# Kernel optimization log

Hardware: AMD Instinct MI355X
Metric: run time of the kernel (lower is better)

## Reference

```python
import jax, jax.numpy as jnp
import numpy as np

NEG_SLOPE = 0.2  # PyG GATConv default negative_slope


def gat_conv(x, edge_index, W, att_src, att_dst, bias):
    """PyG-style GATConv (concat heads, add_self_loops=True, eval mode).
    x: [N, F_in], edge_index: [2, E] (row 0 = src j, row 1 = dst i).
    W: [F_in, H*C], att_src/att_dst: [H, C], bias: [H*C].
    """
    N = x.shape[0]
    H, C = att_src.shape
    loops = jnp.arange(N, dtype=edge_index.dtype)
    src = jnp.concatenate([edge_index[0], loops])  # [E+N]
    dst = jnp.concatenate([edge_index[1], loops])
    h = (x @ W).reshape(N, H, C)                              # [N,H,C]
    a_src = jnp.einsum('nhc,hc->nh', h, att_src)              # [N,H]
    a_dst = jnp.einsum('nhc,hc->nh', h, att_dst)
    alpha = jax.nn.leaky_relu(a_src[src] + a_dst[dst], NEG_SLOPE)  # [E+N,H]
    # segment softmax over edges sharing the same destination node
    m = jax.ops.segment_max(alpha, dst, num_segments=N)       # [N,H]
    e = jnp.exp(alpha - jax.lax.stop_gradient(m)[dst])
    denom = jax.ops.segment_sum(e, dst, num_segments=N)       # [N,H]
    a = e / (denom[dst] + 1e-16)                              # [E+N,H]
    msg = h[src] * a[:, :, None]                              # [E+N,H,C]
    out = jax.ops.segment_sum(msg, dst, num_segments=N)       # [N,H,C]
    return out.reshape(N, H * C) + bias


def setup_inputs() -> dict:
    key = jax.random.key(0)
    ks = jax.random.split(key, 10)
    N, F, NC, C1, H1 = 50000, 128, 40, 16, 8
    E = 800000
    x = jax.random.normal(ks[0], (N, F), dtype=jnp.float32)
    edge_index = jax.random.randint(ks[1], (2, E), 0, N, dtype=jnp.int64)
    s1 = 1.0 / np.sqrt(F)
    W1 = jax.random.uniform(ks[2], (F, H1 * C1), jnp.float32, -s1, s1)
    att_src1 = jax.random.uniform(ks[3], (H1, C1), jnp.float32, -1.0, 1.0) * s1
    att_dst1 = jax.random.uniform(ks[4], (H1, C1), jnp.float32, -1.0, 1.0) * s1
    bias1 = jnp.zeros((H1 * C1,), jnp.float32)
    s2 = 1.0 / np.sqrt(H1 * C1)
    W2 = jax.random.uniform(ks[5], (H1 * C1, NC), jnp.float32, -s2, s2)
    att_src2 = jax.random.uniform(ks[6], (1, NC), jnp.float32, -1.0, 1.0) * s2
    att_dst2 = jax.random.uniform(ks[7], (1, NC), jnp.float32, -1.0, 1.0) * s2
    bias2 = jnp.zeros((NC,), jnp.float32)
    return {"x": x, "edge_index": edge_index, "W1": W1, "att_src1": att_src1,
            "att_dst1": att_dst1, "bias1": bias1, "W2": W2, "att_src2": att_src2,
            "att_dst2": att_dst2, "bias2": bias2}


def reference(x, edge_index, W1, att_src1, att_dst1, bias1, W2, att_src2, att_dst2, bias2):
    h = gat_conv(x, edge_index, W1, att_src1, att_dst1, bias1)   # [N, 128]
    # dropout in eval mode = identity
    out = gat_conv(h, edge_index, W2, att_src2, att_dst2, bias2)  # [N, 40]
    return out
```

## Files before the change

kernel.cpp:

```cpp
#include <hip/hip_runtime.h>
#include <hip/hip_bf16.h>
#include <math.h>

#define NEG_SLOPE 0.2f

typedef __bf16 bf16x8 __attribute__((ext_vector_type(8)));
typedef float f32x4 __attribute__((ext_vector_type(4)));

__device__ __forceinline__ float lrelu(float x) { return x > 0.f ? x : NEG_SLOPE * x; }

__device__ __forceinline__ unsigned int pack_bf2(float a, float b) {
    unsigned int ua = __float_as_uint(a);
    ua = (ua + 0x7fffu + ((ua >> 16) & 1u)) >> 16;
    unsigned int ub = __float_as_uint(b);
    ub = (ub + 0x7fffu + ((ub >> 16) & 1u)) & 0xffff0000u;
    return ua | ub;
}
__device__ __forceinline__ unsigned short f2bfu(float f) {
    unsigned int ua = __float_as_uint(f);
    return (unsigned short)((ua + 0x7fffu + ((ua >> 16) & 1u)) >> 16);
}
__device__ __forceinline__ float bf_lo(unsigned int u) { return __uint_as_float(u << 16); }
__device__ __forceinline__ float bf_hi(unsigned int u) { return __uint_as_float(u & 0xffff0000u); }

__global__ __launch_bounds__(256) void k_hist(const int* __restrict__ ei, int E, int N,
                                              int* __restrict__ cnt, int* __restrict__ rank) {
    int e = blockIdx.x * 256 + threadIdx.x;
    if (e >= E + N) return;
    int d = (e < E) ? ei[E + e] : (e - E);
    rank[e] = atomicAdd(&cnt[d], 1);
}

__global__ __launch_bounds__(256) void k_scan_part(const int* __restrict__ cnt, int N,
                                                   int* __restrict__ psum) {
    __shared__ int sh[256];
    int t = threadIdx.x;
    int base = blockIdx.x * 1024 + t * 4;
    int tl = 0;
#pragma unroll
    for (int j = 0; j < 4; ++j) tl += (base + j < N) ? cnt[base + j] : 0;
    sh[t] = tl; __syncthreads();
    for (int off = 128; off > 0; off >>= 1) {
        if (t < off) sh[t] += sh[t + off];
        __syncthreads();
    }
    if (t == 0) psum[blockIdx.x] = sh[0];
}

__global__ __launch_bounds__(256) void k_scan_mid(int* __restrict__ psum, int nb) {
    __shared__ int sh[256];
    int t = threadIdx.x;
    int v = (t < nb) ? psum[t] : 0;
    sh[t] = v; __syncthreads();
    for (int off = 1; off < 256; off <<= 1) {
        int a = (t >= off) ? sh[t - off] : 0;
        __syncthreads();
        sh[t] += a;
        __syncthreads();
    }
    psum[t] = sh[t] - v;
}

__global__ __launch_bounds__(256) void k_scan_add(const int* __restrict__ cnt, int N,
                                                  const int* __restrict__ psum,
                                                  int* __restrict__ rowptr) {
    __shared__ int sh[256];
    int t = threadIdx.x;
    int base = blockIdx.x * 1024 + t * 4;
    int c[4]; int tl = 0;
#pragma unroll
    for (int j = 0; j < 4; ++j) { c[j] = (base + j < N) ? cnt[base + j] : 0; tl += c[j]; }
    sh[t] = tl; __syncthreads();
    for (int off = 1; off < 256; off <<= 1) {
        int a = (t >= off) ? sh[t - off] : 0;
        __syncthreads();
        sh[t] += a;
        __syncthreads();
    }
    int run = psum[blockIdx.x] + (sh[t] - tl);
#pragma unroll
    for (int j = 0; j < 4; ++j) {
        if (base + j < N) { rowptr[base + j] = run; run += c[j]; }
    }
}

__global__ __launch_bounds__(256) void k_scatter(const int* __restrict__ ei, int E, int N,
                                                 const int* __restrict__ rowptr,
                                                 const int* __restrict__ rank,
                                                 int* __restrict__ col) {
    int e = blockIdx.x * 256 + threadIdx.x;
    if (e >= E + N) return;
    int s, d;
    if (e < E) { s = ei[e]; d = ei[E + e]; } else { s = d = e - E; }
    col[rowptr[d] + rank[e]] = s;
}

__global__ __launch_bounds__(256) void k_wpack(const float* __restrict__ W,
                                               bf16x8* __restrict__ Wp) {
    int idx = blockIdx.x * 256 + threadIdx.x;
    if (idx >= 2048) return;
    int n = idx & 15, quad = (idx >> 4) & 3, c = (idx >> 6) & 3, ct = idx >> 8;
    bf16x8 v;
#pragma unroll
    for (int j = 0; j < 8; ++j)
        v[j] = (__bf16)W[(c * 32 + quad * 8 + j) * 128 + ct * 16 + n];
    Wp[idx] = v;
}

__global__ __launch_bounds__(256) void k_gemm1(const float* __restrict__ x,
                                               const bf16x8* __restrict__ Wp,
                                               const float* __restrict__ att_s,
                                               const float* __restrict__ att_d,
                                               unsigned short* __restrict__ h1A,
                                               unsigned short* __restrict__ h1B,
                                               float* __restrict__ a_src,
                                               float* __restrict__ a_dst, int N) {
    int t = threadIdx.x;
    int w = t >> 6, lane = t & 63, quad = lane >> 4, n16 = lane & 15;
    int row0 = blockIdx.x * 64 + w * 16;
    int arow = row0 + n16; if (arow >= N) arow = N - 1;
    const float* px = x + (size_t)arow * 128;

    bf16x8 ah[4], al[4];
#pragma unroll
    for (int c = 0; c < 4; ++c) {
        float4 v0 = *(const float4*)&px[c * 32 + quad * 8];
        float4 v1 = *(const float4*)&px[c * 32 + quad * 8 + 4];
        float xf[8] = {v0.x, v0.y, v0.z, v0.w, v1.x, v1.y, v1.z, v1.w};
#pragma unroll
        for (int j = 0; j < 8; ++j) {
            __bf16 hi = (__bf16)xf[j];
            ah[c][j] = hi;
            al[c][j] = (__bf16)(xf[j] - (float)hi);
        }
    }

    f32x4 acc[8];
#pragma unroll
    for (int ct = 0; ct < 8; ++ct) acc[ct] = (f32x4){0.f, 0.f, 0.f, 0.f};

    const uint4* wp4 = (const uint4*)Wp;
#pragma unroll
    for (int ct = 0; ct < 8; ++ct) {
#pragma unroll
        for (int c = 0; c < 4; ++c) {
            union { uint4 u; bf16x8 b; } bu;
            bu.u = wp4[((ct * 4 + c) * 4 + quad) * 16 + n16];
            acc[ct] = __builtin_amdgcn_mfma_f32_16x16x32_bf16(ah[c], bu.b, acc[ct], 0, 0, 0);
            acc[ct] = __builtin_amdgcn_mfma_f32_16x16x32_bf16(al[c], bu.b, acc[ct], 0, 0, 0);
        }
    }

    float asv[8], adv[8];
#pragma unroll
    for (int ct = 0; ct < 8; ++ct) {
        asv[ct] = att_s[ct * 16 + n16];
        adv[ct] = att_d[ct * 16 + n16];
    }
    int nodeb = row0 + quad * 4;
#pragma unroll
    for (int ct = 0; ct < 8; ++ct) {
        unsigned short* hp = (ct < 4) ? h1A : h1B;
        int chl = (ct & 3) * 16 + n16;
#pragma unroll
        for (int reg = 0; reg < 4; ++reg) {
            int node = nodeb + reg;
            float hv = acc[ct][reg];
            float ps = hv * asv[ct];
            float pd = hv * adv[ct];
#pragma unroll
            for (int m = 1; m < 16; m <<= 1) {
                ps += __shfl_xor(ps, m);
                pd += __shfl_xor(pd, m);
            }
            if (node < N) {
                hp[(size_t)node * 64 + chl] = f2bfu(hv);
                if (n16 == 0) {
                    a_src[(size_t)node * 8 + ct] = ps;
                    a_dst[(size_t)node * 8 + ct] = pd;
                }
            }
        }
    }
}

__global__ __launch_bounds__(256) void k_aggr1(const int* __restrict__ rowptr,
                                               const int* __restrict__ cnt,
                                               const int* __restrict__ col,
                                               const float* __restrict__ a_src,
                                               const float* __restrict__ a_dst,
                                               const unsigned int* __restrict__ hp,
                                               const float* __restrict__ bias1,
                                               float* __restrict__ out1, int N, int p) {
    __shared__ float evs[4][2][128];
    __shared__ int   cls[4][2][32];
    int t = threadIdx.x;
    int w = t >> 6;
    int lane = t & 63;
    int half = lane >> 5;
    int u = lane & 31;
    int node = blockIdx.x * 8 + w * 2 + half;
    bool nv = (node < N);
    int nodec = nv ? node : (N - 1);
    int beg = rowptr[nodec];
    int deg = nv ? cnt[nodec] : 0;
    int degO = __shfl_xor(deg, 32);
    int degmax = (deg > degO) ? deg : degO;
    if (degmax <= 0) return;

    int hh = u >> 3;
    float4 ad4 = *(const float4*)&a_dst[(size_t)nodec * 8 + p * 4];

    float* myev = &evs[w][half][0];
    int*   mycl = &cls[w][half][0];

    float den = 0.f, n0 = 0.f, n1 = 0.f;
    int c = 0;
    while (c < degmax) {
        int slot = c + u;
        int slotc = (slot < deg) ? slot : (deg - 1);
        if (slotc < 0) slotc = 0;
        int su = col[beg + slotc];
        float4 as4 = *(const float4*)&a_src[(size_t)su * 8 + p * 4];
        bool valid = (slot < deg);
        float e0 = valid ? __expf(lrelu(as4.x + ad4.x)) : 0.f;
        float e1 = valid ? __expf(lrelu(as4.y + ad4.y)) : 0.f;
        float e2 = valid ? __expf(lrelu(as4.z + ad4.z)) : 0.f;
        float e3 = valid ? __expf(lrelu(as4.w + ad4.w)) : 0.f;
        *(float4*)&myev[u * 4] = make_float4(e0, e1, e2, e3);
        mycl[u] = su;

        int ccm = degmax - c; ccm = (ccm < 32) ? ccm : 32;
        int sP = mycl[0];
        unsigned int uP = hp[sP * 32 + u];
        for (int i = 0; i < ccm; ++i) {
            int in = (i + 1 < ccm) ? (i + 1) : i;
            int sN = mycl[in];
            unsigned int uN = hp[sN * 32 + u];
            float ev = myev[i * 4 + hh];
            den += ev;
            n0 = fmaf(ev, bf_lo(uP), n0);
            n1 = fmaf(ev, bf_hi(uP), n1);
            uP = uN;
        }
        c += 32;
    }
    if (nv) {
        float inv = 1.f / (den + 1e-16f);
        int ch = p * 64 + 2 * u;
        float2 b = *(const float2*)&bias1[ch];
        float2 o = make_float2(fmaf(n0, inv, b.x), fmaf(n1, inv, b.y));
        *(float2*)&out1[(size_t)node * 128 + ch] = o;
    }
}

__global__ __launch_bounds__(256) void k_gemm2(const float* __restrict__ out1,
                                               const float* __restrict__ W2,
                                               const float* __restrict__ att_s2,
                                               const float* __restrict__ att_d2,
                                               unsigned int* __restrict__ h2b,
                                               float* __restrict__ a_src2,
                                               float* __restrict__ a_dst2, int N) {
    __shared__ float Ws[128 * 40];
    int t = threadIdx.x;
    for (int i = t * 4; i < 128 * 40; i += 256 * 4)
        *(float4*)&Ws[i] = *(const float4*)&W2[i];
    __syncthreads();
    int n = blockIdx.x * 256 + t;
    if (n >= N) return;

    float acc[40];
#pragma unroll
    for (int c = 0; c < 40; ++c) acc[c] = 0.f;

    for (int k0 = 0; k0 < 128; k0 += 4) {
        float4 v = *(const float4*)&out1[(size_t)n * 128 + k0];
        float xj[4] = {v.x, v.y, v.z, v.w};
#pragma unroll
        for (int j = 0; j < 4; ++j) {
            float xb = xj[j];
#pragma unroll
            for (int c0 = 0; c0 < 40; c0 += 4) {
                float4 wv = *(const float4*)&Ws[(k0 + j) * 40 + c0];
                acc[c0 + 0] = fmaf(xb, wv.x, acc[c0 + 0]);
                acc[c0 + 1] = fmaf(xb, wv.y, acc[c0 + 1]);
                acc[c0 + 2] = fmaf(xb, wv.z, acc[c0 + 2]);
                acc[c0 + 3] = fmaf(xb, wv.w, acc[c0 + 3]);
            }
        }
    }
    float s2 = 0.f, d2 = 0.f;
#pragma unroll
    for (int c = 0; c < 40; ++c) {
        s2 = fmaf(acc[c], att_s2[c], s2);
        d2 = fmaf(acc[c], att_d2[c], d2);
    }
    unsigned int p[20];
#pragma unroll
    for (int j = 0; j < 20; ++j) p[j] = pack_bf2(acc[2 * j], acc[2 * j + 1]);
#pragma unroll
    for (int j = 0; j < 5; ++j)
        *(uint4*)&h2b[(size_t)n * 20 + 4 * j] = make_uint4(p[4 * j], p[4 * j + 1], p[4 * j + 2], p[4 * j + 3]);
    a_src2[n] = s2;
    a_dst2[n] = d2;
}

__global__ __launch_bounds__(256) void k_aggr2(const int* __restrict__ rowptr,
                                               const int* __restrict__ cnt,
                                               const int* __restrict__ col,
                                               const float* __restrict__ a_src,
                                               const float* __restrict__ a_dst,
                                               const unsigned int* __restrict__ h2b,
                                               const float* __restrict__ bias2,
                                               float* __restrict__ out, int N) {
    __shared__ float evs[4][2][32];
    __shared__ int   cls[4][2][32];
    int t = threadIdx.x;
    int w = t >> 6;
    int lane = t & 63;
    int half = lane >> 5;
    int u = lane & 31;
    int node = blockIdx.x * 8 + w * 2 + half;
    bool nv = (node < N);
    int nodec = nv ? node : (N - 1);
    int beg = rowptr[nodec];
    int deg = nv ? cnt[nodec] : 0;
    int degO = __shfl_xor(deg, 32);
    int degmax = (deg > degO) ? deg : degO;
    if (degmax <= 0) return;

    int ucl = (u < 20) ? u : 19;
    float ad = a_dst[nodec];
    float* myev = &evs[w][half][0];
    int*   mycl = &cls[w][half][0];

    float den = 0.f, a0 = 0.f, a1 = 0.f;
    int c = 0;
    while (c < degmax) {
        int slot = c + u;
        int slotc = (slot < deg) ? slot : (deg - 1);
        if (slotc < 0) slotc = 0;
        int su = col[beg + slotc];
        float ev = (slot < deg) ? __expf(lrelu(a_src[su] + ad)) : 0.f;
        myev[u] = ev;
        mycl[u] = su;

        int ccm = degmax - c; ccm = (ccm < 32) ? ccm : 32;
        int sP = mycl[0];
        unsigned int uP = h2b[sP * 20 + ucl];
        for (int i = 0; i < ccm; ++i) {
            int in = (i + 1 < ccm) ? (i + 1) : i;
            int sN = mycl[in];
            unsigned int uN = h2b[sN * 20 + ucl];
            float evv = myev[i];
            den += evv;
            a0 = fmaf(evv, bf_lo(uP), a0);
            a1 = fmaf(evv, bf_hi(uP), a1);
            uP = uN;
        }
        c += 32;
    }
    if (nv && u < 20) {
        float inv = 1.f / (den + 1e-16f);
        float2 b = *(const float2*)&bias2[2 * u];
        float2 o = make_float2(fmaf(a0, inv, b.x), fmaf(a1, inv, b.y));
        *(float2*)&out[(size_t)node * 40 + 2 * u] = o;
    }
}

extern "C" void kernel_launch(void* const* d_in, const int* in_sizes, int n_in,
                              void* d_out, int out_size, void* d_ws, size_t ws_size,
                              hipStream_t stream) {
    const float* x   = (const float*)d_in[0];
    const int*   ei  = (const int*)d_in[1];
    const float* W1  = (const float*)d_in[2];
    const float* as1 = (const float*)d_in[3];
    const float* ad1 = (const float*)d_in[4];
    const float* b1  = (const float*)d_in[5];
    const float* W2  = (const float*)d_in[6];
    const float* as2 = (const float*)d_in[7];
    const float* ad2 = (const float*)d_in[8];
    const float* b2  = (const float*)d_in[9];

    int N = in_sizes[0] / 128;
    int E = in_sizes[1] / 2;
    int EN = E + N;
    size_t Np = (size_t)((N + 3) & ~3);
    size_t ENp = ((size_t)EN + 3) & ~3;

    float* ws = (float*)d_ws;
    float* out1    = ws; ws += Np * 128;
    unsigned int* h1A = (unsigned int*)ws; ws += Np * 32;
    unsigned int* h1Bp = (unsigned int*)ws; ws += Np * 32;
    unsigned int* h2b = (unsigned int*)ws; ws += Np * 20;
    float* a_src1  = ws; ws += Np * 8;
    float* a_dst1  = ws; ws += Np * 8;
    float* a_src2v = ws; ws += Np;
    float* a_dst2v = ws; ws += Np;
    bf16x8* Wp = (bf16x8*)ws; ws += 2048 * 4;
    int* cnt    = (int*)ws; ws += Np;
    int* rowptr = (int*)ws; ws += Np;
    int* psum   = (int*)ws; ws += 256;
    int* col    = (int*)ws; ws += ENp;
    int* rank   = (int*)ws; ws += ENp;

    int nb = (N + 1023) / 1024;

    hipMemsetAsync(cnt, 0, (size_t)N * sizeof(int), stream);
    k_wpack<<<8, 256, 0, stream>>>(W1, Wp);
    k_hist<<<(EN + 255) / 256, 256, 0, stream>>>(ei, E, N, cnt, rank);
    k_scan_part<<<nb, 256, 0, stream>>>(cnt, N, psum);
    k_scan_mid<<<1, 256, 0, stream>>>(psum, nb);
    k_scan_add<<<nb, 256, 0, stream>>>(cnt, N, psum, rowptr);
    k_scatter<<<(EN + 255) / 256, 256, 0, stream>>>(ei, E, N, rowptr, rank, col);

    k_gemm1<<<(N + 63) / 64, 256, 0, stream>>>(x, Wp, as1, ad1,
                                               (unsigned short*)h1A, (unsigned short*)h1Bp,
                                               a_src1, a_dst1, N);
    int nag = (N + 7) / 8;
    k_aggr1<<<nag, 256, 0, stream>>>(rowptr, cnt, col, a_src1, a_dst1, h1A, b1, out1, N, 0);
    k_aggr1<<<nag, 256, 0, stream>>>(rowptr, cnt, col, a_src1, a_dst1, h1Bp, b1, out1, N, 1);
    k_gemm2<<<(N + 255) / 256, 256, 0, stream>>>(out1, W2, as2, ad2, h2b, a_src2v, a_dst2v, N);
    k_aggr2<<<nag, 256, 0, stream>>>(rowptr, cnt, col, a_src2v, a_dst2v, h2b, b2, (float*)d_out, N);
}
```

Baseline: 266.1 us.

## Use bf16 MFMA with hi/lo split for second-layer GEMM

```diff
diff --git a/kernel.cpp b/kernel.cpp
--- a/kernel.cpp
+++ b/kernel.cpp
@@ -9,16 +9,12 @@
 
 __device__ __forceinline__ float lrelu(float x) { return x > 0.f ? x : NEG_SLOPE * x; }
 
-__device__ __forceinline__ unsigned int pack_bf2(float a, float b) {
-    unsigned int ua = __float_as_uint(a);
-    ua = (ua + 0x7fffu + ((ua >> 16) & 1u)) >> 16;
-    unsigned int ub = __float_as_uint(b);
-    ub = (ub + 0x7fffu + ((ub >> 16) & 1u)) & 0xffff0000u;
-    return ua | ub;
-}
 __device__ __forceinline__ unsigned short f2bfu(float f) {
     unsigned int ua = __float_as_uint(f);
     return (unsigned short)((ua + 0x7fffu + ((ua >> 16) & 1u)) >> 16);
+}
+__device__ __forceinline__ float bfu2f(unsigned short u) {
+    return __uint_as_float(((unsigned int)u) << 16);
 }
 __device__ __forceinline__ float bf_lo(unsigned int u) { return __uint_as_float(u << 16); }
 __device__ __forceinline__ float bf_hi(unsigned int u) { return __uint_as_float(u & 0xffff0000u); }
@@ -105,6 +101,19 @@
     for (int j = 0; j < 8; ++j)
         v[j] = (__bf16)W[(c * 32 + quad * 8 + j) * 128 + ct * 16 + n];
     Wp[idx] = v;
+}
+
+__global__ __launch_bounds__(256) void k_wpack2(const float* __restrict__ W2,
+                                                bf16x8* __restrict__ W2p) {
+    int idx = blockIdx.x * 256 + threadIdx.x;
+    if (idx >= 768) return;
+    int n = idx & 15, quad = (idx >> 4) & 3, c = (idx >> 6) & 3, ct = idx >> 8;
+    int colc = ct * 16 + n;
+    bf16x8 v;
+#pragma unroll
+    for (int j = 0; j < 8; ++j)
+        v[j] = (colc < 40) ? (__bf16)W2[(c * 32 + quad * 8 + j) * 40 + colc] : (__bf16)0.f;
+    W2p[idx] = v;
 }
 
 __global__ __launch_bounds__(256) void k_gemm1(const float* __restrict__ x,
@@ -191,7 +200,8 @@
                                                const float* __restrict__ a_dst,
                                                const unsigned int* __restrict__ hp,
                                                const float* __restrict__ bias1,
-                                               float* __restrict__ out1, int N, int p) {
+                                               unsigned int* __restrict__ out1h,
+                                               unsigned int* __restrict__ out1l, int N, int p) {
     __shared__ float evs[4][2][128];
     __shared__ int   cls[4][2][32];
     int t = threadIdx.x;
@@ -249,60 +259,85 @@
         float inv = 1.f / (den + 1e-16f);
         int ch = p * 64 + 2 * u;
         float2 b = *(const float2*)&bias1[ch];
-        float2 o = make_float2(fmaf(n0, inv, b.x), fmaf(n1, inv, b.y));
-        *(float2*)&out1[(size_t)node * 128 + ch] = o;
-    }
-}
-
-__global__ __launch_bounds__(256) void k_gemm2(const float* __restrict__ out1,
-                                               const float* __restrict__ W2,
+        float o0 = fmaf(n0, inv, b.x), o1 = fmaf(n1, inv, b.y);
+        unsigned short h0 = f2bfu(o0), h1 = f2bfu(o1);
+        float l0 = o0 - bfu2f(h0), l1 = o1 - bfu2f(h1);
+        size_t idx = (size_t)node * 64 + p * 32 + u;
+        out1h[idx] = (unsigned int)h0 | ((unsigned int)h1 << 16);
+        out1l[idx] = (unsigned int)f2bfu(l0) | ((unsigned int)f2bfu(l1) << 16);
+    }
+}
+
+__global__ __launch_bounds__(256) void k_gemm2(const unsigned int* __restrict__ out1h,
+                                               const unsigned int* __restrict__ out1l,
+                                               const bf16x8* __restrict__ W2p,
                                                const float* __restrict__ att_s2,
                                                const float* __restrict__ att_d2,
-                                               unsigned int* __restrict__ h2b,
+                                               unsigned short* __restrict__ h2s,
                                                float* __restrict__ a_src2,
                                                float* __restrict__ a_dst2, int N) {
-    __shared__ float Ws[128 * 40];
-    int t = threadIdx.x;
-    for (int i = t * 4; i < 128 * 40; i += 256 * 4)
-        *(float4*)&Ws[i] = *(const float4*)&W2[i];
-    __syncthreads();
-    int n = blockIdx.x * 256 + t;
-    if (n >= N) return;
-
-    float acc[40];
-#pragma unroll
-    for (int c = 0; c < 40; ++c) acc[c] = 0.f;
-
-    for (int k0 = 0; k0 < 128; k0 += 4) {
-        float4 v = *(const float4*)&out1[(size_t)n * 128 + k0];
-        float xj[4] = {v.x, v.y, v.z, v.w};
-#pragma unroll
-        for (int j = 0; j < 4; ++j) {
-            float xb = xj[j];
-#pragma unroll
-            for (int c0 = 0; c0 < 40; c0 += 4) {
-                float4 wv = *(const float4*)&Ws[(k0 + j) * 40 + c0];
-                acc[c0 + 0] = fmaf(xb, wv.x, acc[c0 + 0]);
-                acc[c0 + 1] = fmaf(xb, wv.y, acc[c0 + 1]);
-                acc[c0 + 2] = fmaf(xb, wv.z, acc[c0 + 2]);
-                acc[c0 + 3] = fmaf(xb, wv.w, acc[c0 + 3]);
-            }
-        }
-    }
-    float s2 = 0.f, d2 = 0.f;
-#pragma unroll
-    for (int c = 0; c < 40; ++c) {
-        s2 = fmaf(acc[c], att_s2[c], s2);
-        d2 = fmaf(acc[c], att_d2[c], d2);
-    }
-    unsigned int p[20];
-#pragma unroll
-    for (int j = 0; j < 20; ++j) p[j] = pack_bf2(acc[2 * j], acc[2 * j + 1]);
-#pragma unroll
-    for (int j = 0; j < 5; ++j)
-        *(uint4*)&h2b[(size_t)n * 20 + 4 * j] = make_uint4(p[4 * j], p[4 * j + 1], p[4 * j + 2], p[4 * j + 3]);
-    a_src2[n] = s2;
-    a_dst2[n] = d2;
+    int t = threadIdx.x;
+    int w = t >> 6, lane = t & 63, quad = lane >> 4, n16 = lane & 15;
+    int row0 = blockIdx.x * 64 + w * 16;
+    int arow = row0 + n16; if (arow >= N) arow = N - 1;
+
+    bf16x8 ah[4], al[4];
+#pragma unroll
+    for (int c = 0; c < 4; ++c) {
+        size_t base = (size_t)arow * 64 + (c * 32 + quad * 8) / 2;
+        union { uint4 u; bf16x8 b; } hu, lu;
+        hu.u = *(const uint4*)&out1h[base];
+        lu.u = *(const uint4*)&out1l[base];
+        ah[c] = hu.b;
+        al[c] = lu.b;
+    }
+
+    f32x4 acc[3];
+#pragma unroll
+    for (int ct = 0; ct < 3; ++ct) acc[ct] = (f32x4){0.f, 0.f, 0.f, 0.f};
+
+    const uint4* wp4 = (const uint4*)W2p;
+#pragma unroll
+    for (int ct = 0; ct < 3; ++ct) {
+#pragma unroll
+        for (int c = 0; c < 4; ++c) {
+            union { uint4 u; bf16x8 b; } bu;
+            bu.u = wp4[((ct * 4 + c) * 4 + quad) * 16 + n16];
+            acc[ct] = __builtin_amdgcn_mfma_f32_16x16x32_bf16(ah[c], bu.b, acc[ct], 0, 0, 0);
+            acc[ct] = __builtin_amdgcn_mfma_f32_16x16x32_bf16(al[c], bu.b, acc[ct], 0, 0, 0);
+        }
+    }
+
+    float asv[3], adv[3];
+#pragma unroll
+    for (int ct = 0; ct < 3; ++ct) {
+        int ch = ct * 16 + n16;
+        asv[ct] = (ch < 40) ? att_s2[ch] : 0.f;
+        adv[ct] = (ch < 40) ? att_d2[ch] : 0.f;
+    }
+    int nodeb = row0 + quad * 4;
+#pragma unroll
+    for (int reg = 0; reg < 4; ++reg) {
+        int node = nodeb + reg;
+        float ps = 0.f, pd = 0.f;
+#pragma unroll
+        for (int ct = 0; ct < 3; ++ct) {
+            float hv = acc[ct][reg];
+            ps = fmaf(hv, asv[ct], ps);
+            pd = fmaf(hv, adv[ct], pd);
+            int ch = ct * 16 + n16;
+            if (node < N && ch < 40) h2s[(size_t)node * 40 + ch] = f2bfu(hv);
+        }
+#pragma unroll
+        for (int m = 1; m < 16; m <<= 1) {
+            ps += __shfl_xor(ps, m);
+            pd += __shfl_xor(pd, m);
+        }
+        if (node < N && n16 == 0) {
+            a_src2[node] = ps;
+            a_dst2[node] = pd;
+        }
+    }
 }
 
 __global__ __launch_bounds__(256) void k_aggr2(const int* __restrict__ rowptr,
@@ -389,7 +424,8 @@
     size_t ENp = ((size_t)EN + 3) & ~3;
 
     float* ws = (float*)d_ws;
-    float* out1    = ws; ws += Np * 128;
+    unsigned int* out1h = (unsigned int*)ws; ws += Np * 64;
+    unsigned int* out1l = (unsigned int*)ws; ws += Np * 64;
     unsigned int* h1A = (unsigned int*)ws; ws += Np * 32;
     unsigned int* h1Bp = (unsigned int*)ws; ws += Np * 32;
     unsigned int* h2b = (unsigned int*)ws; ws += Np * 20;
@@ -397,7 +433,8 @@
     float* a_dst1  = ws; ws += Np * 8;
     float* a_src2v = ws; ws += Np;
     float* a_dst2v = ws; ws += Np;
-    bf16x8* Wp = (bf16x8*)ws; ws += 2048 * 4;
+    bf16x8* Wp  = (bf16x8*)ws; ws += 2048 * 4;
+    bf16x8* W2p = (bf16x8*)ws; ws += 768 * 4;
     int* cnt    = (int*)ws; ws += Np;
     int* rowptr = (int*)ws; ws += Np;
     int* psum   = (int*)ws; ws += 256;
@@ -408,6 +445,7 @@
 
     hipMemsetAsync(cnt, 0, (size_t)N * sizeof(int), stream);
     k_wpack<<<8, 256, 0, stream>>>(W1, Wp);
+    k_wpack2<<<3, 256, 0, stream>>>(W2, W2p);
     k_hist<<<(EN + 255) / 256, 256, 0, stream>>>(ei, E, N, cnt, rank);
     k_scan_part<<<nb, 256, 0, stream>>>(cnt, N, psum);
     k_scan_mid<<<1, 256, 0, stream>>>(psum, nb);
@@ -418,8 +456,9 @@
                                                (unsigned short*)h1A, (unsigned short*)h1Bp,
                                                a_src1, a_dst1, N);
     int nag = (N + 7) / 8;
-    k_aggr1<<<nag, 256, 0, stream>>>(rowptr, cnt, col, a_src1, a_dst1, h1A, b1, out1, N, 0);
-    k_aggr1<<<nag, 256, 0, stream>>>(rowptr, cnt, col, a_src1, a_dst1, h1Bp, b1, out1, N, 1);
-    k_gemm2<<<(N + 255) / 256, 256, 0, stream>>>(out1, W2, as2, ad2, h2b, a_src2v, a_dst2v, N);
+    k_aggr1<<<nag, 256, 0, stream>>>(rowptr, cnt, col, a_src1, a_dst1, h1A, b1, out1h, out1l, N, 0);
+    k_aggr1<<<nag, 256, 0, stream>>>(rowptr, cnt, col, a_src1, a_dst1, h1Bp, b1, out1h, out1l, N, 1);
+    k_gemm2<<<(N + 63) / 64, 256, 0, stream>>>(out1h, out1l, W2p, as2, ad2,
+                                               (unsigned short*)h2b, a_src2v, a_dst2v, N);
     k_aggr2<<<nag, 256, 0, stream>>>(rowptr, cnt, col, a_src2v, a_dst2v, h2b, b2, (float*)d_out, N);
 }
```

Result: faster. 249.4 us (-6.3%).
